# Optimization experiments

Measured on AMD Instinct MI355X. Metric: run time of the kernel, lower is better.

## Reference

```python
import jax, jax.numpy as jnp
import numpy as np

N = 262144
H = 128
NB = 3  # alpha, xp, yp branches


def _lin_init(key, out_d, in_d, shape):
    bound = 1.0 / np.sqrt(in_d)
    return jax.random.uniform(key, shape, jnp.float32, -bound, bound)


def setup_inputs() -> dict:
    key = jax.random.key(0)
    ks = jax.random.split(key, 9)
    t = jax.random.normal(ks[0], (N,), jnp.float32)
    W1 = _lin_init(ks[1], H, 1, (NB, H, 1))
    b1 = _lin_init(ks[2], H, 1, (NB, H))
    W2 = _lin_init(ks[3], H, H, (NB, H, H))
    b2 = _lin_init(ks[4], H, H, (NB, H))
    W3 = _lin_init(ks[5], H, H, (NB, H, H))
    b3 = _lin_init(ks[6], H, H, (NB, H))
    W4 = _lin_init(ks[7], 1, H, (NB, 1, H))
    b4 = _lin_init(ks[8], 1, H, (NB, 1))
    return {"t": t, "W1": W1, "b1": b1, "W2": W2, "b2": b2,
            "W3": W3, "b3": b3, "W4": W4, "b4": b4}


def _mlp(t, w1, c1, w2, c2, w3, c3, w4, c4):
    # t: [N]; one branch: 1 -> H -> H -> H -> 1 with relu on hidden layers
    h = jax.nn.relu(t[:, None] * w1[:, 0][None, :] + c1)  # [N, H]
    h = jax.nn.relu(h @ w2.T + c2)                        # [N, H]
    h = jax.nn.relu(h @ w3.T + c3)                        # [N, H]
    return (h @ w4.T + c4)[:, 0]                          # [N]


def _post(v, dt, neg):
    # dt is d(v)/dt per element (= the torch double-backward result)
    s = -1.0 if neg else 1.0
    dsign = s * jnp.sign(v - v[0]) * dt
    d0 = jnp.where(dsign[1] >= 0, jnp.abs(dt[0:1]), -jnp.abs(dt[0:1]))
    dsign = jnp.concatenate([d0, dsign[1:]])
    vv = s * jnp.abs(v - v[0])
    return vv, dsign


def reference(t, W1, b1, W2, b2, W3, b3, W4, b4):
    ones = jnp.ones_like(t)

    def branch(w1, c1, w2, c2, w3, c3, w4, c4):
        # value and analytic d/dt via forward-mode JVP (tangent of t is 1)
        return jax.jvp(lambda tt: _mlp(tt, w1, c1, w2, c2, w3, c3, w4, c4),
                       (t,), (ones,))

    vals, dts = jax.vmap(branch)(W1, b1, W2, b2, W3, b3, W4, b4)  # [3, N] each
    alpha, da = _post(vals[0], dts[0], False)
    xp, dx = _post(vals[1], dts[1], True)
    yp, dy = _post(vals[2], dts[2], False)
    return (alpha, xp, yp, da, dx, dy)
```

## Files before the change

kernel.cpp:

```cpp
#include <hip/hip_runtime.h>
#include <math.h>

#define N_ELEM 262144
#define HDIM 128
#define M_TILE 64
#define DEADBAND 2e-5f
#define GAPBAND 4e-5f
#define REFNOISE 1e-6
#define THR_FRAC 0.0198f
#define EPS_1 2e-6f
#define EPS_A 1e-5f
#define CMAX 9.0e-3f
#define CAP 16384

typedef __attribute__((ext_vector_type(8))) short bf16x8;
typedef __attribute__((ext_vector_type(4))) short bf16x4;
typedef __attribute__((ext_vector_type(4))) float f32x4;

static __device__ __forceinline__ unsigned short f2bf(float x) {
    unsigned u = __float_as_uint(x);
    unsigned r = u + 0x7FFF + ((u >> 16) & 1);
    return (unsigned short)(r >> 16);
}
static __device__ __forceinline__ float bf2f(unsigned short h) {
    return __uint_as_float(((unsigned)h) << 16);
}

static __device__ __forceinline__ void tsplit3(float x, unsigned short& h0,
                                               unsigned short& h1, unsigned short& h2) {
    unsigned u0 = __float_as_uint(x);
    h0 = (unsigned short)(u0 >> 16);
    float r1 = x - __uint_as_float(u0 & 0xFFFF0000u);
    unsigned u1 = __float_as_uint(r1);
    h1 = (unsigned short)(u1 >> 16);
    float r2 = r1 - __uint_as_float(u1 & 0xFFFF0000u);
    h2 = f2bf(r2);
}


__global__ void k_prep(const float* __restrict__ W2, const float* __restrict__ W3,
                       unsigned short* __restrict__ Wb0, unsigned short* __restrict__ Wb1,
                       unsigned short* __restrict__ Wb2) {
    int g = blockIdx.x * 256 + threadIdx.x;
    const float* src = (g >= 49152) ? W3 : W2;
    int r = (g >= 49152) ? g - 49152 : g;
    float w = src[r];
    unsigned short h0 = f2bf(w);
    float r1 = w - bf2f(h0);
    unsigned short h1 = f2bf(r1);
    Wb0[g] = h0; Wb1[g] = h1; Wb2[g] = f2bf(r1 - bf2f(h1));
}

__global__ __launch_bounds__(256, 2) void k_mlp(
    const float* __restrict__ t,  const float* __restrict__ W1,
    const float* __restrict__ b1, const float* __restrict__ b2,
    const float* __restrict__ b3, const float* __restrict__ W4,
    const float* __restrict__ b4,
    const unsigned short* __restrict__ Wb0, const unsigned short* __restrict__ Wb1,
    const unsigned short* __restrict__ Wb2,
    float* __restrict__ vf, float* __restrict__ out,
    unsigned* __restrict__ cnt, unsigned* __restrict__ list)
{
    __shared__ __align__(16) unsigned short Bv0[64][136];
    __shared__ __align__(16) unsigned short Bv1[64][136];
    __shared__ __align__(16) unsigned short Bv2[64][136];
    __shared__ __align__(16) unsigned short Bt0[64][136];
    __shared__ unsigned char flg[64];

    const int tid  = threadIdx.x;
    const int wave = tid >> 6;
    const int lane = tid & 63;
    const int quad = lane >> 4;
    const int n16  = lane & 15;
    const int b    = blockIdx.y;
    const int e0   = blockIdx.x * M_TILE;

    if (tid < 64) flg[tid] = 0;
    __syncthreads();

    {
        const int m  = tid >> 2;
        const int kb = (tid & 3) * 32;
        float tval = t[e0 + m];
        const float* W1p = W1 + b * 128 + kb;
        const float* b1p = b1 + b * 128 + kb;
        unsigned char f = 0;
        #pragma unroll
        for (int kh = 0; kh < 4; ++kh) {
            f32x4 wA = *(const f32x4*)(W1p + kh * 8);
            f32x4 wB = *(const f32x4*)(W1p + kh * 8 + 4);
            f32x4 cA = *(const f32x4*)(b1p + kh * 8);
            f32x4 cB = *(const f32x4*)(b1p + kh * 8 + 4);
            bf16x8 rv0, rv1, rv2, rt0;
            #pragma unroll
            for (int kk = 0; kk < 8; ++kk) {
                float w1 = (kk < 4) ? wA[kk] : wB[kk - 4];
                float bb = (kk < 4) ? cA[kk] : cB[kk - 4];
                float pre = fmaf(tval, w1, bb);
                if (fabsf(pre) < EPS_1) f = 1;
                float hv = pre > 0.f ? pre : 0.f;
                float ht = pre > 0.f ? w1 : 0.f;
                unsigned short a0, a1, a2;
                tsplit3(hv, a0, a1, a2);
                rv0[kk] = (short)a0;
                rv1[kk] = (short)a1;
                rv2[kk] = (short)a2;
                rt0[kk] = (short)f2bf(ht);
            }
            *(bf16x8*)&Bv0[m][kb + kh * 8] = rv0;
            *(bf16x8*)&Bv1[m][kb + kh * 8] = rv1;
            *(bf16x8*)&Bv2[m][kb + kh * 8] = rv2;
            *(bf16x8*)&Bt0[m][kb + kh * 8] = rt0;
        }
        if (f) flg[m] = 1;
    }
    __syncthreads();

    const int jt0 = wave * 2;
    #pragma unroll 1
    for (int lay = 0; lay < 2; ++lay) {
        const float* bias = (lay ? b3 : b2) + b * 128;

        const unsigned short* A0[2];
        const unsigned short* A1[2];
        const unsigned short* A2[2];
        f32x4 bias4[2];
        #pragma unroll
        for (int jj = 0; jj < 2; ++jj) {
            const int row = ((jt0 + jj) << 4) + n16;
            const int off = ((lay * 3 + b) << 14) + (row << 7);
            A0[jj] = Wb0 + off;
            A1[jj] = Wb1 + off;
            A2[jj] = Wb2 + off;
            bias4[jj] = *(const f32x4*)(bias + ((jt0 + jj) << 4) + quad * 4);
        }

        f32x4 z = {0.f, 0.f, 0.f, 0.f};
        f32x4 accv[2][4] = {{z, z, z, z}, {z, z, z, z}};
        f32x4 acct[2][4] = {{z, z, z, z}, {z, z, z, z}};

        #pragma unroll
        for (int ks = 0; ks < 4; ++ks) {
            const int koff = ks * 32 + quad * 8;
            bf16x8 w0[2], w1[2], w2[2];
            #pragma unroll
            for (int jj = 0; jj < 2; ++jj) {
                w0[jj] = *(const bf16x8*)(A0[jj] + koff);
                w1[jj] = *(const bf16x8*)(A1[jj] + koff);
                w2[jj] = *(const bf16x8*)(A2[jj] + koff);
            }
            #pragma unroll
            for (int mm = 0; mm < 4; ++mm) {
                const int mrow = mm * 16 + n16;
                bf16x8 a0 = *(const bf16x8*)&Bv0[mrow][koff];
                bf16x8 a1 = *(const bf16x8*)&Bv1[mrow][koff];
                bf16x8 a2 = *(const bf16x8*)&Bv2[mrow][koff];
                bf16x8 c0 = *(const bf16x8*)&Bt0[mrow][koff];
                #pragma unroll
                for (int jj = 0; jj < 2; ++jj) {
                    accv[jj][mm] = __builtin_amdgcn_mfma_f32_16x16x32_bf16(w0[jj], a2, accv[jj][mm], 0, 0, 0);
                    accv[jj][mm] = __builtin_amdgcn_mfma_f32_16x16x32_bf16(w1[jj], a1, accv[jj][mm], 0, 0, 0);
                    accv[jj][mm] = __builtin_amdgcn_mfma_f32_16x16x32_bf16(w2[jj], a0, accv[jj][mm], 0, 0, 0);
                    accv[jj][mm] = __builtin_amdgcn_mfma_f32_16x16x32_bf16(w0[jj], a1, accv[jj][mm], 0, 0, 0);
                    accv[jj][mm] = __builtin_amdgcn_mfma_f32_16x16x32_bf16(w1[jj], a0, accv[jj][mm], 0, 0, 0);
                    accv[jj][mm] = __builtin_amdgcn_mfma_f32_16x16x32_bf16(w0[jj], a0, accv[jj][mm], 0, 0, 0);
                    acct[jj][mm] = __builtin_amdgcn_mfma_f32_16x16x32_bf16(w1[jj], c0, acct[jj][mm], 0, 0, 0);
                    acct[jj][mm] = __builtin_amdgcn_mfma_f32_16x16x32_bf16(w0[jj], c0, acct[jj][mm], 0, 0, 0);
                }
            }
        }
        __syncthreads();

        #pragma unroll
        for (int jj = 0; jj < 2; ++jj) {
            const int jcol = ((jt0 + jj) << 4) + quad * 4;
            #pragma unroll
            for (int mm = 0; mm < 4; ++mm) {
                const int m = mm * 16 + n16;
                bf16x4 p0, p1, p2, q0;
                #pragma unroll
                for (int r = 0; r < 4; ++r) {
                    float pre = accv[jj][mm][r] + bias4[jj][r];
                    float tp  = acct[jj][mm][r];
                    if (fabsf(pre) < EPS_A) flg[m] = 1;
                    float hv = pre > 0.f ? pre : 0.f;
                    float ht = pre > 0.f ? tp : 0.f;
                    unsigned short a0, a1, a2;
                    tsplit3(hv, a0, a1, a2);
                    p0[r] = (short)a0;
                    p1[r] = (short)a1;
                    p2[r] = (short)a2;
                    q0[r] = (short)f2bf(ht);
                }
                *(bf16x4*)&Bv0[m][jcol] = p0;
                *(bf16x4*)&Bv1[m][jcol] = p1;
                *(bf16x4*)&Bv2[m][jcol] = p2;
                *(bf16x4*)&Bt0[m][jcol] = q0;
            }
        }
        __syncthreads();
    }

    {
        const int m  = tid >> 2;
        const int tp = tid & 3;
        const int jb = tp * 32;
        const float* W4p = W4 + b * 128 + jb;
        float pv = 0.f, pt = 0.f;
        #pragma unroll
        for (int c = 0; c < 4; ++c) {
            bf16x8 q0 = *(bf16x8*)&Bv0[m][jb + c * 8];
            bf16x8 q1 = *(bf16x8*)&Bv1[m][jb + c * 8];
            bf16x8 q2 = *(bf16x8*)&Bv2[m][jb + c * 8];
            bf16x8 s0 = *(bf16x8*)&Bt0[m][jb + c * 8];
            f32x4 wA = *(const f32x4*)(W4p + c * 8);
            f32x4 wB = *(const f32x4*)(W4p + c * 8 + 4);
            #pragma unroll
            for (int l = 0; l < 8; ++l) {
                float hv = (bf2f((unsigned short)q0[l]) + bf2f((unsigned short)q1[l]))
                           + bf2f((unsigned short)q2[l]);
                float ht = bf2f((unsigned short)s0[l]);
                float w = (l < 4) ? wA[l] : wB[l - 4];
                pv = fmaf(hv, w, pv);
                pt = fmaf(ht, w, pt);
            }
        }
        pv += __shfl_xor(pv, 1); pv += __shfl_xor(pv, 2);
        pt += __shfl_xor(pt, 1); pt += __shfl_xor(pt, 2);
        if (tp == 0) {
            vf[b * N_ELEM + e0 + m] = pv + b4[b];
            out[3 * N_ELEM + b * N_ELEM + e0 + m] = pt;
        }
    }

    if (tid < 64 && flg[tid]) {
        unsigned idx = atomicAdd(cnt, 1u);
        if (idx < CAP) list[idx] = (unsigned)(b * N_ELEM + e0 + tid);
    }
}


__global__ void k_exact01(
    const float* __restrict__ t,  const float* __restrict__ W1,
    const float* __restrict__ b1, const float* __restrict__ W2,
    const float* __restrict__ b2, const float* __restrict__ W3,
    const float* __restrict__ b3, const float* __restrict__ W4,
    const float* __restrict__ b4, double* __restrict__ sc)
{
    __shared__ double h[128], h2[128], red[128];
    int j = threadIdx.x;
    for (int b = 0; b < 3; ++b)
        for (int e = 0; e < 2; ++e) {
            double tv = (double)t[e];
            double pre = fma(tv, (double)W1[b * 128 + j], (double)b1[b * 128 + j]);
            h[j] = pre > 0.0 ? pre : 0.0;
            __syncthreads();
            {
                const float* W = W2 + b * 16384 + j * 128;
                double acc = (double)b2[b * 128 + j];
                for (int k0 = 0; k0 < 128; k0 += 4) {
                    f32x4 wq = *(const f32x4*)(W + k0);
                    #pragma unroll
                    for (int kk = 0; kk < 4; ++kk)
                        acc = fma(h[k0 + kk], (double)wq[kk], acc);
                }
                h2[j] = acc > 0.0 ? acc : 0.0;
            }
            __syncthreads();
            {
                const float* W = W3 + b * 16384 + j * 128;
                double acc = (double)b3[b * 128 + j];
                for (int k0 = 0; k0 < 128; k0 += 4) {
                    f32x4 wq = *(const f32x4*)(W + k0);
                    #pragma unroll
                    for (int kk = 0; kk < 4; ++kk)
                        acc = fma(h2[k0 + kk], (double)wq[kk], acc);
                }
                h[j] = acc > 0.0 ? acc : 0.0;
            }
            __syncthreads();
            red[j] = h[j] * (double)W4[b * 128 + j];
            __syncthreads();
            for (int s = 64; s > 0; s >>= 1) {
                if (j < s) red[j] += red[j + s];
                __syncthreads();
            }
            if (j == 0) sc[b * 4 + e] = red[0] + (double)b4[b];
            __syncthreads();
        }
}

__global__ void k_gmax_flag(const float* __restrict__ vf,
                            const float* __restrict__ out,
                            const double* __restrict__ sc,
                            unsigned* __restrict__ gm,
                            unsigned* __restrict__ cnt,
                            unsigned* __restrict__ list) {
    __shared__ unsigned red[4];
    int g = blockIdx.x * 256 + threadIdx.x;
    int b = g / N_ELEM;
    float v0 = (float)sc[b * 4];
    float gap = fabsf(vf[g] - v0);
    float dt  = fabsf(out[3 * N_ELEM + g]);
    if (gap < GAPBAND) {
        unsigned idx = atomicAdd(cnt, 1u);
        if (idx < CAP) list[idx] = (unsigned)g;
    }
    unsigned v = __float_as_uint(fmaxf(gap, dt));
    #pragma unroll
    for (int s = 1; s < 64; s <<= 1) {
        unsigned o = (unsigned)__shfl_xor((int)v, s);
        v = v > o ? v : o;
    }
    int wave = threadIdx.x >> 6;
    if ((threadIdx.x & 63) == 0) red[wave] = v;
    __syncthreads();
    if (threadIdx.x == 0) {
        unsigned m = red[0];
        #pragma unroll
        for (int w = 1; w < 4; ++w) m = m > red[w] ? m : red[w];
        atomicMax(gm, m);
    }
}

__global__ __launch_bounds__(128) void k_fix(
    const float* __restrict__ t,  const float* __restrict__ W1,
    const float* __restrict__ b1, const float* __restrict__ W2,
    const float* __restrict__ b2, const float* __restrict__ W3,
    const float* __restrict__ b3, const float* __restrict__ W4,
    const float* __restrict__ b4,
    const unsigned* __restrict__ cnt, const unsigned* __restrict__ list,
    float* __restrict__ out, float* __restrict__ vf,
    double* __restrict__ vex, float* __restrict__ fixdt)
{
    __shared__ double hT[128], hA[128], hB[128];
    __shared__ float  tT[128], tA[128], tB[128];
    __shared__ double nhT[128], nhA[128], nhB[128];
    __shared__ float  ntT[128], ntA[128], ntB[128];
    unsigned c = *cnt; if (c > CAP) c = CAP;
    unsigned n = blockIdx.x;
    if (n >= c) return;
    unsigned g = list[n];
    int b = g / N_ELEM;
    int i = g - b * N_ELEM;
    int j = threadIdx.x;

    double tv = (double)t[i];
    float  w1 = W1[b * 128 + j];
    double pre = fma(tv, (double)w1, (double)b1[b * 128 + j]);
    bool amb = fabs(pre) < (double)EPS_1;
    bool mT = pre > 0.0;
    bool mA = amb ? false : mT;
    bool mB = amb ? true  : mT;
    hT[j] = mT ? pre : 0.0;  tT[j] = mT ? w1 : 0.f;
    hA[j] = mA ? pre : 0.0;  tA[j] = mA ? w1 : 0.f;
    hB[j] = mB ? pre : 0.0;  tB[j] = mB ? w1 : 0.f;
    __syncthreads();

    #pragma unroll 1
    for (int layer = 0; layer < 2; ++layer) {
        const float* W = (layer ? W3 : W2) + b * 16384 + j * 128;
        double bb = (double)((layer ? b3 : b2)[b * 128 + j]);
        double pT = bb, pA = bb, pB = bb;
        float  zT = 0.f, zA = 0.f, zB = 0.f;
        for (int k0 = 0; k0 < 128; k0 += 4) {
            f32x4 wq = *(const f32x4*)(W + k0);
            #pragma unroll
            for (int kk = 0; kk < 4; ++kk) {
                int k = k0 + kk;
                float wf = wq[kk];
                double wd = (double)wf;
                pT = fma(hT[k], wd, pT); zT = fmaf(tT[k], wf, zT);
                pA = fma(hA[k], wd, pA); zA = fmaf(tA[k], wf, zA);
                pB = fma(hB[k], wd, pB); zB = fmaf(tB[k], wf, zB);
            }
        }
        bool mTl  = pT > 0.0;
        bool ambl = (fabs(pA) < (double)EPS_A) || (fabs(pB) < (double)EPS_A);
        bool mAl  = ambl ? false : (pA > 0.0);
        bool mBl  = ambl ? true  : (pB > 0.0);
        nhT[j] = mTl ? pT : 0.0;  ntT[j] = mTl ? zT : 0.f;
        nhA[j] = mAl ? pA : 0.0;  ntA[j] = mAl ? zA : 0.f;
        nhB[j] = mBl ? pB : 0.0;  ntB[j] = mBl ? zB : 0.f;
        __syncthreads();
        hT[j] = nhT[j]; tT[j] = ntT[j];
        hA[j] = nhA[j]; tA[j] = ntA[j];
        hB[j] = nhB[j]; tB[j] = ntB[j];
        __syncthreads();
    }

    if (j == 0) {
        double vT = 0.0; float dT = 0.f, dA = 0.f, dB = 0.f;
        for (int k0 = 0; k0 < 128; k0 += 4) {
            f32x4 wq = *(const f32x4*)(W4 + b * 128 + k0);
            #pragma unroll
            for (int kk = 0; kk < 4; ++kk) {
                int k = k0 + kk;
                float w4 = wq[kk];
                vT = fma(hT[k], (double)w4, vT);
                dT = fmaf(tT[k], w4, dT);
                dA = fmaf(tA[k], w4, dA);
                dB = fmaf(tB[k], w4, dB);
            }
        }
        vT += (double)b4[b];
        float delta = dB - dA;
        float dtfix = (fabsf(delta) < CMAX) ? 0.5f * (dA + dB) : dT;
        out[3 * N_ELEM + g] = dtfix;
        fixdt[n] = dtfix;
        vex[n]   = vT;
        vf[g]    = (float)vT;
    }
}

__global__ void k_scal(const float* __restrict__ out, double* __restrict__ sc) {
    int b = threadIdx.x;
    if (b < 3) {
        sc[b * 4 + 2] = (double)out[3 * N_ELEM + b * N_ELEM];
        sc[b * 4 + 3] = (double)out[3 * N_ELEM + b * N_ELEM + 1];
    }
}

__global__ void k_post(const float* __restrict__ vf,
                       float* __restrict__ out,
                       const double* __restrict__ sc,
                       const unsigned* __restrict__ gm) {
    int g = blockIdx.x * 256 + threadIdx.x;
    int b = g / N_ELEM;
    int i = g - b * N_ELEM;
    float s = (b == 1) ? -1.f : 1.f;
    float thr = THR_FRAC * __uint_as_float(*gm);

    float v0 = (float)sc[b * 4];
    float v  = vf[b * N_ELEM + i];
    float dt = out[3 * N_ELEM + b * N_ELEM + i];

    float d   = v - v0;
    float gap = fabsf(d);
    float ds;
    if (i == 0) {
        double v1  = sc[b * 4 + 1];
        double dt0 = sc[b * 4 + 2];
        double dt1 = sc[b * 4 + 3];
        double d1  = v1 - sc[b * 4];
        double sg1 = (d1 > 0.0) ? 1.0 : ((d1 < 0.0) ? -1.0 : 0.0);
        double ds1 = (double)s * sg1 * dt1;
        ds = (float)((ds1 >= 0.0) ? fabs(dt0) : -fabs(dt0));
        if (fabs(dt0) < (double)thr) ds = 0.f;
        gap = 0.f;
    } else {
        float sgn = (d > 0.f) ? 1.f : ((d < 0.f) ? -1.f : 0.f);
        ds = s * sgn * dt;
        if (gap < DEADBAND && fabsf(dt) < thr) ds = 0.f;
    }
    out[b * N_ELEM + i]              = s * gap;
    out[3 * N_ELEM + b * N_ELEM + i] = ds;
}

__global__ void k_fix2(const unsigned* __restrict__ cnt,
                       const unsigned* __restrict__ list,
                       const double* __restrict__ vex,
                       const float* __restrict__ fixdt,
                       const double* __restrict__ sc,
                       const unsigned* __restrict__ gm,
                       float* __restrict__ out) {
    unsigned c = *cnt; if (c > CAP) c = CAP;
    unsigned n = blockIdx.x * 64 + threadIdx.x;
    if (n >= c) return;
    unsigned g = list[n];
    int b = g / N_ELEM;
    int i = g - b * N_ELEM;
    if (i == 0) return;
    double s = (b == 1) ? -1.0 : 1.0;
    double gapd = vex[n] - sc[b * 4];
    float  dt   = fixdt[n];
    float  thr  = THR_FRAC * __uint_as_float(*gm);
    double sgn = (gapd > 0.0) ? 1.0 : ((gapd < 0.0) ? -1.0 : 0.0);
    float ds = (float)(s * sgn) * dt;
    if (fabs(gapd) < REFNOISE && fabsf(dt) < thr) ds = 0.f;
    out[b * N_ELEM + i]              = (float)(s * fabs(gapd));
    out[3 * N_ELEM + b * N_ELEM + i] = ds;
}

extern "C" void kernel_launch(void* const* d_in, const int* in_sizes, int n_in,
                              void* d_out, int out_size, void* d_ws, size_t ws_size,
                              hipStream_t stream) {
    const float* t  = (const float*)d_in[0];
    const float* W1 = (const float*)d_in[1];
    const float* b1 = (const float*)d_in[2];
    const float* W2 = (const float*)d_in[3];
    const float* b2 = (const float*)d_in[4];
    const float* W3 = (const float*)d_in[5];
    const float* b3 = (const float*)d_in[6];
    const float* W4 = (const float*)d_in[7];
    const float* b4 = (const float*)d_in[8];
    float* out = (float*)d_out;
    char* ws   = (char*)d_ws;
    unsigned short* Wb0 = (unsigned short*)ws;
    unsigned short* Wb1 = (unsigned short*)(ws + 196608);
    float*    vf    = (float*)(ws + 393216);
    double*   sc    = (double*)(ws + 3538944);
    unsigned* gm    = (unsigned*)(ws + 3539040);
    unsigned* cnt   = (unsigned*)(ws + 3539044);
    unsigned* list  = (unsigned*)(ws + 3539048);
    double*   vex   = (double*)(ws + 3604592);
    float*    fixdt = (float*)(ws + 3735664);
    unsigned short* Wb2 = (unsigned short*)(ws + 3801200);

    hipMemsetAsync(gm, 0, 8, stream);
    k_prep<<<384, 256, 0, stream>>>(W2, W3, Wb0, Wb1, Wb2);
    k_mlp<<<dim3(N_ELEM / M_TILE, 3), 256, 0, stream>>>(t, W1, b1, b2, b3, W4, b4,
                                                        Wb0, Wb1, Wb2, vf, out, cnt, list);
    k_exact01<<<1, 128, 0, stream>>>(t, W1, b1, W2, b2, W3, b3, W4, b4, sc);
    k_gmax_flag<<<(3 * N_ELEM) / 256, 256, 0, stream>>>(vf, out, sc, gm, cnt, list);
    k_fix<<<CAP, 128, 0, stream>>>(t, W1, b1, W2, b2, W3, b3, W4, b4,
                                   cnt, list, out, vf, vex, fixdt);
    k_scal<<<1, 64, 0, stream>>>(out, sc);
    k_post<<<(3 * N_ELEM) / 256, 256, 0, stream>>>(vf, out, sc, gm);
    k_fix2<<<CAP / 64, 64, 0, stream>>>(cnt, list, vex, fixdt, sc, gm, out);
}
```

Baseline: 1.152 ms.

## Switch hidden-layer GEMMs to 32x32x16 MFMA with XOR-swizzled LDS activations

The hidden-layer matmuls move from 16x16x32 bf16 MFMA tiles (each wave owning 32 output columns across 4 row tiles) to 32x32x16 MFMA tiles (each wave owning 32 output columns across 2 row tiles of 32). The LDS activation buffers lose their row padding and use an XOR swizzle on the column index to avoid bank conflicts under the new access pattern. The aim is fewer MFMA issues, fewer weight loads per wave and better LDS reuse per instruction, at the cost of larger accumulators (register pressure at 2 blocks/SM) and more index arithmetic.

```diff
diff --git a/kernel.cpp b/kernel.cpp
--- a/kernel.cpp
+++ b/kernel.cpp
@@ -16,6 +16,7 @@
 typedef __attribute__((ext_vector_type(8))) short bf16x8;
 typedef __attribute__((ext_vector_type(4))) short bf16x4;
 typedef __attribute__((ext_vector_type(4))) float f32x4;
+typedef __attribute__((ext_vector_type(16))) float f32x16;
 
 static __device__ __forceinline__ unsigned short f2bf(float x) {
     unsigned u = __float_as_uint(x);
@@ -61,17 +62,17 @@
     float* __restrict__ vf, float* __restrict__ out,
     unsigned* __restrict__ cnt, unsigned* __restrict__ list)
 {
-    __shared__ __align__(16) unsigned short Bv0[64][136];
-    __shared__ __align__(16) unsigned short Bv1[64][136];
-    __shared__ __align__(16) unsigned short Bv2[64][136];
-    __shared__ __align__(16) unsigned short Bt0[64][136];
+    __shared__ __align__(16) unsigned short Bv0[64 * 128];
+    __shared__ __align__(16) unsigned short Bv1[64 * 128];
+    __shared__ __align__(16) unsigned short Bv2[64 * 128];
+    __shared__ __align__(16) unsigned short Bt0[64 * 128];
     __shared__ unsigned char flg[64];
 
     const int tid  = threadIdx.x;
     const int wave = tid >> 6;
     const int lane = tid & 63;
-    const int quad = lane >> 4;
-    const int n16  = lane & 15;
+    const int l31  = lane & 31;
+    const int half = lane >> 5;
     const int b    = blockIdx.y;
     const int e0   = blockIdx.x * M_TILE;
 
@@ -81,6 +82,8 @@
     {
         const int m  = tid >> 2;
         const int kb = (tid & 3) * 32;
+        const int sw = (m & 7) << 3;
+        const int mb = m << 7;
         float tval = t[e0 + m];
         const float* W1p = W1 + b * 128 + kb;
         const float* b1p = b1 + b * 128 + kb;
@@ -107,81 +110,76 @@
                 rv2[kk] = (short)a2;
                 rt0[kk] = (short)f2bf(ht);
             }
-            *(bf16x8*)&Bv0[m][kb + kh * 8] = rv0;
-            *(bf16x8*)&Bv1[m][kb + kh * 8] = rv1;
-            *(bf16x8*)&Bv2[m][kb + kh * 8] = rv2;
-            *(bf16x8*)&Bt0[m][kb + kh * 8] = rt0;
+            const int idx = mb + ((kb + kh * 8) ^ sw);
+            *(bf16x8*)&Bv0[idx] = rv0;
+            *(bf16x8*)&Bv1[idx] = rv1;
+            *(bf16x8*)&Bv2[idx] = rv2;
+            *(bf16x8*)&Bt0[idx] = rt0;
         }
         if (f) flg[m] = 1;
     }
     __syncthreads();
 
-    const int jt0 = wave * 2;
+    const int swz = (l31 & 7) << 3;
     #pragma unroll 1
     for (int lay = 0; lay < 2; ++lay) {
         const float* bias = (lay ? b3 : b2) + b * 128;
 
-        const unsigned short* A0[2];
-        const unsigned short* A1[2];
-        const unsigned short* A2[2];
-        f32x4 bias4[2];
-        #pragma unroll
-        for (int jj = 0; jj < 2; ++jj) {
-            const int row = ((jt0 + jj) << 4) + n16;
-            const int off = ((lay * 3 + b) << 14) + (row << 7);
-            A0[jj] = Wb0 + off;
-            A1[jj] = Wb1 + off;
-            A2[jj] = Wb2 + off;
-            bias4[jj] = *(const f32x4*)(bias + ((jt0 + jj) << 4) + quad * 4);
-        }
-
-        f32x4 z = {0.f, 0.f, 0.f, 0.f};
-        f32x4 accv[2][4] = {{z, z, z, z}, {z, z, z, z}};
-        f32x4 acct[2][4] = {{z, z, z, z}, {z, z, z, z}};
-
-        #pragma unroll
-        for (int ks = 0; ks < 4; ++ks) {
-            const int koff = ks * 32 + quad * 8;
-            bf16x8 w0[2], w1[2], w2[2];
-            #pragma unroll
-            for (int jj = 0; jj < 2; ++jj) {
-                w0[jj] = *(const bf16x8*)(A0[jj] + koff);
-                w1[jj] = *(const bf16x8*)(A1[jj] + koff);
-                w2[jj] = *(const bf16x8*)(A2[jj] + koff);
-            }
-            #pragma unroll
-            for (int mm = 0; mm < 4; ++mm) {
-                const int mrow = mm * 16 + n16;
-                bf16x8 a0 = *(const bf16x8*)&Bv0[mrow][koff];
-                bf16x8 a1 = *(const bf16x8*)&Bv1[mrow][koff];
-                bf16x8 a2 = *(const bf16x8*)&Bv2[mrow][koff];
-                bf16x8 c0 = *(const bf16x8*)&Bt0[mrow][koff];
-                #pragma unroll
-                for (int jj = 0; jj < 2; ++jj) {
-                    accv[jj][mm] = __builtin_amdgcn_mfma_f32_16x16x32_bf16(w0[jj], a2, accv[jj][mm], 0, 0, 0);
-                    accv[jj][mm] = __builtin_amdgcn_mfma_f32_16x16x32_bf16(w1[jj], a1, accv[jj][mm], 0, 0, 0);
-                    accv[jj][mm] = __builtin_amdgcn_mfma_f32_16x16x32_bf16(w2[jj], a0, accv[jj][mm], 0, 0, 0);
-                    accv[jj][mm] = __builtin_amdgcn_mfma_f32_16x16x32_bf16(w0[jj], a1, accv[jj][mm], 0, 0, 0);
-                    accv[jj][mm] = __builtin_amdgcn_mfma_f32_16x16x32_bf16(w1[jj], a0, accv[jj][mm], 0, 0, 0);
-                    accv[jj][mm] = __builtin_amdgcn_mfma_f32_16x16x32_bf16(w0[jj], a0, accv[jj][mm], 0, 0, 0);
-                    acct[jj][mm] = __builtin_amdgcn_mfma_f32_16x16x32_bf16(w1[jj], c0, acct[jj][mm], 0, 0, 0);
-                    acct[jj][mm] = __builtin_amdgcn_mfma_f32_16x16x32_bf16(w0[jj], c0, acct[jj][mm], 0, 0, 0);
-                }
+        const int wrow = (wave << 5) + l31;
+        const int woff = ((lay * 3 + b) << 14) + (wrow << 7) + (half << 3);
+        const unsigned short* pW0 = Wb0 + woff;
+        const unsigned short* pW1 = Wb1 + woff;
+        const unsigned short* pW2 = Wb2 + woff;
+
+        f32x4 bias4[4];
+        #pragma unroll
+        for (int g = 0; g < 4; ++g)
+            bias4[g] = *(const f32x4*)(bias + (wave << 5) + (g << 3) + (half << 2));
+
+        f32x16 accv[2], acct[2];
+        #pragma unroll
+        for (int mm = 0; mm < 2; ++mm) {
+            #pragma unroll
+            for (int r = 0; r < 16; ++r) { accv[mm][r] = 0.f; acct[mm][r] = 0.f; }
+        }
+
+        #pragma unroll
+        for (int ks = 0; ks < 8; ++ks) {
+            bf16x8 w0 = *(const bf16x8*)(pW0 + (ks << 4));
+            bf16x8 w1 = *(const bf16x8*)(pW1 + (ks << 4));
+            bf16x8 w2 = *(const bf16x8*)(pW2 + (ks << 4));
+            const int cx = ((ks << 4) + (half << 3)) ^ swz;
+            #pragma unroll
+            for (int mm = 0; mm < 2; ++mm) {
+                const int idx = (mm << 12) + (l31 << 7) + cx;
+                bf16x8 a0 = *(const bf16x8*)&Bv0[idx];
+                bf16x8 a1 = *(const bf16x8*)&Bv1[idx];
+                bf16x8 a2 = *(const bf16x8*)&Bv2[idx];
+                bf16x8 c0 = *(const bf16x8*)&Bt0[idx];
+                accv[mm] = __builtin_amdgcn_mfma_f32_32x32x16_bf16(w0, a2, accv[mm], 0, 0, 0);
+                accv[mm] = __builtin_amdgcn_mfma_f32_32x32x16_bf16(w1, a1, accv[mm], 0, 0, 0);
+                accv[mm] = __builtin_amdgcn_mfma_f32_32x32x16_bf16(w2, a0, accv[mm], 0, 0, 0);
+                accv[mm] = __builtin_amdgcn_mfma_f32_32x32x16_bf16(w0, a1, accv[mm], 0, 0, 0);
+                accv[mm] = __builtin_amdgcn_mfma_f32_32x32x16_bf16(w1, a0, accv[mm], 0, 0, 0);
+                accv[mm] = __builtin_amdgcn_mfma_f32_32x32x16_bf16(w0, a0, accv[mm], 0, 0, 0);
+                acct[mm] = __builtin_amdgcn_mfma_f32_32x32x16_bf16(w1, c0, acct[mm], 0, 0, 0);
+                acct[mm] = __builtin_amdgcn_mfma_f32_32x32x16_bf16(w0, c0, acct[mm], 0, 0, 0);
             }
         }
         __syncthreads();
 
         #pragma unroll
-        for (int jj = 0; jj < 2; ++jj) {
-            const int jcol = ((jt0 + jj) << 4) + quad * 4;
-            #pragma unroll
-            for (int mm = 0; mm < 4; ++mm) {
-                const int m = mm * 16 + n16;
+        for (int mm = 0; mm < 2; ++mm) {
+            const int mb = (mm << 12) + (l31 << 7);
+            const int m  = (mm << 5) + l31;
+            #pragma unroll
+            for (int g = 0; g < 4; ++g) {
+                const int jc = (wave << 5) + (g << 3) + (half << 2);
                 bf16x4 p0, p1, p2, q0;
                 #pragma unroll
                 for (int r = 0; r < 4; ++r) {
-                    float pre = accv[jj][mm][r] + bias4[jj][r];
-                    float tp  = acct[jj][mm][r];
+                    float pre = accv[mm][g * 4 + r] + bias4[g][r];
+                    float tp  = acct[mm][g * 4 + r];
                     if (fabsf(pre) < EPS_A) flg[m] = 1;
                     float hv = pre > 0.f ? pre : 0.f;
                     float ht = pre > 0.f ? tp : 0.f;
@@ -192,10 +190,11 @@
                     p2[r] = (short)a2;
                     q0[r] = (short)f2bf(ht);
                 }
-                *(bf16x4*)&Bv0[m][jcol] = p0;
-                *(bf16x4*)&Bv1[m][jcol] = p1;
-                *(bf16x4*)&Bv2[m][jcol] = p2;
-                *(bf16x4*)&Bt0[m][jcol] = q0;
+                const int widx = mb + (jc ^ swz);
+                *(bf16x4*)&Bv0[widx] = p0;
+                *(bf16x4*)&Bv1[widx] = p1;
+                *(bf16x4*)&Bv2[widx] = p2;
+                *(bf16x4*)&Bt0[widx] = q0;
             }
         }
         __syncthreads();
@@ -205,14 +204,17 @@
         const int m  = tid >> 2;
         const int tp = tid & 3;
         const int jb = tp * 32;
+        const int sw = (m & 7) << 3;
+        const int mb = m << 7;
         const float* W4p = W4 + b * 128 + jb;
         float pv = 0.f, pt = 0.f;
         #pragma unroll
         for (int c = 0; c < 4; ++c) {
-            bf16x8 q0 = *(bf16x8*)&Bv0[m][jb + c * 8];
-            bf16x8 q1 = *(bf16x8*)&Bv1[m][jb + c * 8];
-            bf16x8 q2 = *(bf16x8*)&Bv2[m][jb + c * 8];
-            bf16x8 s0 = *(bf16x8*)&Bt0[m][jb + c * 8];
+            const int idx = mb + ((jb + c * 8) ^ sw);
+            bf16x8 q0 = *(bf16x8*)&Bv0[idx];
+            bf16x8 q1 = *(bf16x8*)&Bv1[idx];
+            bf16x8 q2 = *(bf16x8*)&Bv2[idx];
+            bf16x8 s0 = *(bf16x8*)&Bt0[idx];
             f32x4 wA = *(const f32x4*)(W4p + c * 8);
             f32x4 wB = *(const f32x4*)(W4p + c * 8 + 4);
             #pragma unroll
```

After: 1.125 ms. 2.4% less time.
